# Kernel tuning notes

Measured on AMD Instinct MI355X. Metric: run time of the kernel, lower is better.

## Reference

```python
import jax, jax.numpy as jnp
import numpy as np

EPS = 1e-9
# ((top,bottom),(left,right)) zero-pads for the 8 neighbor directions,
# matching torch nn.ZeroPad2d((l,r,t,b)) order gate1..gate8 in the source.
PADS = [((0, 2), (0, 2)), ((0, 2), (1, 1)), ((0, 2), (2, 0)),
        ((1, 1), (0, 2)), ((1, 1), (2, 0)),
        ((2, 0), (0, 2)), ((2, 0), (1, 1)), ((2, 0), (2, 0))]


def _pad8(x):
    # x: (B,H,W) -> (B,8,H+2,W+2): 8 directional zero-padded shifts
    return jnp.stack([jnp.pad(x, ((0, 0), tb, lr)) for tb, lr in PADS], axis=1)


def _affinity_normalization(guidance):
    # guidance: (B,8,H,W) -> gate_wb (B,8,H+2,W+2), gate_sum (B,H,W)
    gate_wb = jnp.stack(
        [jnp.pad(guidance[:, k], ((0, 0), tb, lr)) for k, (tb, lr) in enumerate(PADS)],
        axis=1)
    abs_weight = jnp.sum(jnp.abs(gate_wb), axis=1, keepdims=True)
    gate_wb = gate_wb / (abs_weight + EPS)
    gate_sum = jnp.sum(gate_wb, axis=1)[:, 1:-1, 1:-1]
    return gate_wb, gate_sum


def setup_inputs() -> dict:
    key = jax.random.key(0)
    k1, k2, k3, k4 = jax.random.split(key, 4)
    B, H, W = 2, 384, 1280
    guidance = jax.random.normal(k1, (B, 8, H, W), dtype=jnp.float32)
    blur_depth = jax.random.uniform(k2, (B, 1, H, W), dtype=jnp.float32) * 80.0
    valid = (jax.random.uniform(k3, (B, 1, H, W)) < 0.05).astype(jnp.float32)
    sparse_depth = valid * jax.random.uniform(k4, (B, 1, H, W), dtype=jnp.float32) * 80.0
    return {"guidance": guidance, "blur_depth": blur_depth,
            "sparse_depth": sparse_depth, "prop_time": 24}


def reference(guidance, blur_depth, sparse_depth, prop_time):
    # CSPN affinity-guided iterative propagation (norm_type='8sum')
    gate_wb, gate_sum = _affinity_normalization(guidance)
    raw = blur_depth[:, 0]                       # (B,H,W)
    sparse_mask = jnp.sign(sparse_depth[:, 0])   # (B,H,W), 1 where valid
    d = raw
    for _ in range(prop_time):
        # weighted sum over 8 padded neighbor shifts, then crop halo
        nws = jnp.sum(gate_wb * _pad8(d), axis=1)[:, 1:-1, 1:-1]
        d = (1.0 - gate_sum) * raw + nws
        d = (1.0 - sparse_mask) * d + sparse_mask * raw
    return d  # (B,H,W), matches result_depth.squeeze(1)
```

## Files before the change

### kernel.cpp

```cpp
#include <hip/hip_runtime.h>
#include <hip/hip_fp16.h>

static constexpr int Hh = 384;
static constexpr int Ww = 1280;
static constexpr int HW = Hh * Ww;
static constexpr int NPIX = 2 * HW;
static constexpr int TILE = 32;
static constexpr int S = 6;
static constexpr int R = TILE + 2 * S;
static constexpr int RR = R * R;
static constexpr int ISIDE = R - 2;
static constexpr int NINT = ISIDE * ISIDE;
static constexpr int BLOCK = 256;
static constexpr int PPQ = (RR + BLOCK - 1) / BLOCK;
static constexpr int PPI = (NINT + BLOCK - 1) / BLOCK;
static constexpr int TI = Hh / TILE;
static constexpr int TJ = Ww / TILE;
static constexpr int GRID = 2 * TI * TJ;
static constexpr int NXCD = 8;
static constexpr int CHUNK = GRID / NXCD;
static constexpr float EPSF = 1e-9f;

__device__ __constant__ int DI_c[8] = { 1, 1, 1, 0, 0, -1, -1, -1 };
__device__ __constant__ int DJ_c[8] = { 1, 0, -1, 1, -1, 1, 0, -1 };

__global__ void affinity_norm(const float* __restrict__ g,
                              const float* __restrict__ raw,
                              const float* __restrict__ sparse,
                              __half* __restrict__ wbuf,
                              float* __restrict__ cbuf) {
    int idx = blockIdx.x * blockDim.x + threadIdx.x;
    if (idx >= NPIX) return;
    int b = idx / HW;
    int r = idx - b * HW;
    int i = r / Ww;
    int j = r - i * Ww;

    const float* gb = g + (size_t)b * 8 * HW;
    float v[8];
    float a = EPSF;
#pragma unroll
    for (int k = 0; k < 8; k++) {
        int ii = i + DI_c[k], jj = j + DJ_c[k];
        float gv = 0.0f;
        if (ii >= 0 && ii < Hh && jj >= 0 && jj < Ww)
            gv = gb[k * HW + ii * Ww + jj];
        v[k] = gv;
        a += fabsf(gv);
    }
    float inv = 1.0f / a, gs = 0.0f;
#pragma unroll
    for (int k = 0; k < 8; k++) { v[k] *= inv; gs += v[k]; }

    float rawv = raw[idx];
    bool m = sparse[idx] > 0.0f;
    cbuf[idx] = m ? rawv : (1.0f - gs) * rawv;
    __half wv[8];
#pragma unroll
    for (int k = 0; k < 8; k++) wv[k] = __float2half(m ? 0.0f : v[k]);
    *(float4*)(wbuf + (size_t)idx * 8) = *(const float4*)wv;
}

__global__ __launch_bounds__(BLOCK, 4) void fused_steps(
    const __half* __restrict__ wbuf, const float* __restrict__ cbuf,
    const float* __restrict__ din, float* __restrict__ dout)
{
    __shared__ float sd[2][RR];

    const int tid = threadIdx.x;
    int bx = (blockIdx.x % NXCD) * CHUNK + blockIdx.x / NXCD;
    const int tj = bx % TJ; bx /= TJ;
    const int ti = bx % TI;
    const int b  = bx / TI;
    const int oi = ti * TILE - S;
    const int oj = tj * TILE - S;

#pragma unroll
    for (int q = 0; q < PPQ; q++) {
        int p = tid + q * BLOCK;
        if (p < RR) {
            int ri = p / R, rj = p - ri * R;
            int gic = min(max(oi + ri, 0), Hh - 1);
            int gjc = min(max(oj + rj, 0), Ww - 1);
            float v = din[b * HW + gic * Ww + gjc];
            sd[0][p] = v;
            if (ri == 0 || ri == R - 1 || rj == 0 || rj == R - 1)
                sd[1][p] = v;
        }
    }

    float w[PPI][8];
    float C[PPI];
    int   pp[PPI];
    int   rng[PPI];
#pragma unroll
    for (int q = 0; q < PPI; q++) {
        int pi = tid + q * BLOCK;
        if (pi < NINT) {
            int r0 = pi / ISIDE;
            int ri = 1 + r0, rj = 1 + (pi - r0 * ISIDE);
            int p = ri * R + rj;
            pp[q]  = p;
            rng[q] = min(min(ri, R - 1 - ri), min(rj, R - 1 - rj));
            int gic = min(max(oi + ri, 0), Hh - 1);
            int gjc = min(max(oj + rj, 0), Ww - 1);
            int idx = b * HW + gic * Ww + gjc;
            float4 wv = *(const float4*)(wbuf + (size_t)idx * 8);
            const __half2* wh = (const __half2*)&wv;
            float2 w01 = __half22float2(wh[0]);
            float2 w23 = __half22float2(wh[1]);
            float2 w45 = __half22float2(wh[2]);
            float2 w67 = __half22float2(wh[3]);
            w[q][0] = w01.x; w[q][1] = w01.y; w[q][2] = w23.x; w[q][3] = w23.y;
            w[q][4] = w45.x; w[q][5] = w45.y; w[q][6] = w67.x; w[q][7] = w67.y;
            C[q] = cbuf[idx];
        } else {
            rng[q] = 0;
            pp[q] = 0;
        }
    }
    __syncthreads();

    int cur = 0;
#pragma unroll
    for (int s = 1; s < S; s++) {
        const float* s0 = sd[cur];
        float* s1 = sd[cur ^ 1];
#pragma unroll
        for (int q = 0; q < PPI; q++) {
            if (rng[q] >= s) {
                int p = pp[q];
                float v = C[q]
                    + w[q][0] * s0[p + R + 1] + w[q][1] * s0[p + R]
                    + w[q][2] * s0[p + R - 1] + w[q][3] * s0[p + 1]
                    + w[q][4] * s0[p - 1]     + w[q][5] * s0[p - R + 1]
                    + w[q][6] * s0[p - R]     + w[q][7] * s0[p - R - 1];
                s1[p] = v;
            }
        }
        __syncthreads();
        cur ^= 1;
    }

    const float* s0 = sd[cur];
#pragma unroll
    for (int q = 0; q < PPI; q++) {
        if (rng[q] >= S) {
            int p = pp[q];
            float v = C[q]
                + w[q][0] * s0[p + R + 1] + w[q][1] * s0[p + R]
                + w[q][2] * s0[p + R - 1] + w[q][3] * s0[p + 1]
                + w[q][4] * s0[p - 1]     + w[q][5] * s0[p - R + 1]
                + w[q][6] * s0[p - R]     + w[q][7] * s0[p - R - 1];
            int ri = p / R, rj = p - ri * R;
            dout[b * HW + (oi + ri) * Ww + (oj + rj)] = v;
        }
    }
}

extern "C" void kernel_launch(void* const* d_in, const int* in_sizes, int n_in,
                              void* d_out, int out_size, void* d_ws, size_t ws_size,
                              hipStream_t stream) {
    const float* guidance = (const float*)d_in[0];
    const float* blur     = (const float*)d_in[1];
    const float* sparse   = (const float*)d_in[2];
    float* out = (float*)d_out;

    char* ws = (char*)d_ws;
    float* bufA = (float*)ws;
    float* bufB = bufA + NPIX;
    __half* wbuf = (__half*)(bufB + NPIX);
    float*  cbuf = (float*)(wbuf + (size_t)NPIX * 8);

    const int threads = 256;
    const int blocks = (NPIX + threads - 1) / threads;
    affinity_norm<<<blocks, threads, 0, stream>>>(guidance, blur, sparse, wbuf, cbuf);

    fused_steps<<<GRID, BLOCK, 0, stream>>>(wbuf, cbuf, blur, bufA);
    fused_steps<<<GRID, BLOCK, 0, stream>>>(wbuf, cbuf, bufA, bufB);
    fused_steps<<<GRID, BLOCK, 0, stream>>>(wbuf, cbuf, bufB, bufA);
    fused_steps<<<GRID, BLOCK, 0, stream>>>(wbuf, cbuf, bufA, out);
}
```

Measured before the change: 142.5 us.

## Fuse affinity normalization and all propagation steps into one halo-tiled kernel

Replaces the separate affinity-normalization kernel and four 6-step propagation launches with a single kernel. Each block computes a 64x64 output tile with a 24-pixel halo entirely in shared memory. Each block computes its normalized weights directly from guidance, and it runs all 24 iterations without global intermediate buffers or relaunches. The cost is much more redundant halo compute, 512-thread blocks holding 24 pixels of packed-half weights per thread (heavy register pressure and likely spills), and low occupancy from the roughly 100 KB shared-memory footprint. The XCD block remapping is also dropped.

```diff
diff --git a/kernel.cpp b/kernel.cpp
--- a/kernel.cpp
+++ b/kernel.cpp
@@ -4,137 +4,122 @@
 static constexpr int Hh = 384;
 static constexpr int Ww = 1280;
 static constexpr int HW = Hh * Ww;
-static constexpr int NPIX = 2 * HW;
-static constexpr int TILE = 32;
-static constexpr int S = 6;
-static constexpr int R = TILE + 2 * S;
+static constexpr int TILE = 64;
+static constexpr int T = 24;
+static constexpr int R = TILE + 2 * T;
 static constexpr int RR = R * R;
 static constexpr int ISIDE = R - 2;
 static constexpr int NINT = ISIDE * ISIDE;
-static constexpr int BLOCK = 256;
+static constexpr int BLOCK = 512;
 static constexpr int PPQ = (RR + BLOCK - 1) / BLOCK;
 static constexpr int PPI = (NINT + BLOCK - 1) / BLOCK;
 static constexpr int TI = Hh / TILE;
 static constexpr int TJ = Ww / TILE;
 static constexpr int GRID = 2 * TI * TJ;
-static constexpr int NXCD = 8;
-static constexpr int CHUNK = GRID / NXCD;
 static constexpr float EPSF = 1e-9f;
 
-__device__ __constant__ int DI_c[8] = { 1, 1, 1, 0, 0, -1, -1, -1 };
-__device__ __constant__ int DJ_c[8] = { 1, 0, -1, 1, -1, 1, 0, -1 };
+static constexpr int DI[8] = { 1, 1, 1, 0, 0, -1, -1, -1 };
+static constexpr int DJ[8] = { 1, 0, -1, 1, -1, 1, 0, -1 };
 
-__global__ void affinity_norm(const float* __restrict__ g,
-                              const float* __restrict__ raw,
-                              const float* __restrict__ sparse,
-                              __half* __restrict__ wbuf,
-                              float* __restrict__ cbuf) {
-    int idx = blockIdx.x * blockDim.x + threadIdx.x;
-    if (idx >= NPIX) return;
-    int b = idx / HW;
-    int r = idx - b * HW;
-    int i = r / Ww;
-    int j = r - i * Ww;
-
-    const float* gb = g + (size_t)b * 8 * HW;
-    float v[8];
-    float a = EPSF;
-#pragma unroll
-    for (int k = 0; k < 8; k++) {
-        int ii = i + DI_c[k], jj = j + DJ_c[k];
-        float gv = 0.0f;
-        if (ii >= 0 && ii < Hh && jj >= 0 && jj < Ww)
-            gv = gb[k * HW + ii * Ww + jj];
-        v[k] = gv;
-        a += fabsf(gv);
-    }
-    float inv = 1.0f / a, gs = 0.0f;
-#pragma unroll
-    for (int k = 0; k < 8; k++) { v[k] *= inv; gs += v[k]; }
-
-    float rawv = raw[idx];
-    bool m = sparse[idx] > 0.0f;
-    cbuf[idx] = m ? rawv : (1.0f - gs) * rawv;
-    __half wv[8];
-#pragma unroll
-    for (int k = 0; k < 8; k++) wv[k] = __float2half(m ? 0.0f : v[k]);
-    *(float4*)(wbuf + (size_t)idx * 8) = *(const float4*)wv;
+static __device__ __forceinline__ int iclamp(int v, int lo, int hi) {
+    return min(max(v, lo), hi);
 }
 
-__global__ __launch_bounds__(BLOCK, 4) void fused_steps(
-    const __half* __restrict__ wbuf, const float* __restrict__ cbuf,
-    const float* __restrict__ din, float* __restrict__ dout)
+__global__ __launch_bounds__(BLOCK, 2) void mega(
+    const float* __restrict__ g,
+    const float* __restrict__ blur,
+    const float* __restrict__ sparse,
+    float* __restrict__ out)
 {
     __shared__ float sd[2][RR];
 
     const int tid = threadIdx.x;
-    int bx = (blockIdx.x % NXCD) * CHUNK + blockIdx.x / NXCD;
+    int bx = blockIdx.x;
     const int tj = bx % TJ; bx /= TJ;
     const int ti = bx % TI;
     const int b  = bx / TI;
-    const int oi = ti * TILE - S;
-    const int oj = tj * TILE - S;
+    const int oi = ti * TILE - T;
+    const int oj = tj * TILE - T;
+
+    const float* blurb = blur + (size_t)b * HW;
+    const float* gb    = g    + (size_t)b * 8 * HW;
 
 #pragma unroll
     for (int q = 0; q < PPQ; q++) {
         int p = tid + q * BLOCK;
         if (p < RR) {
             int ri = p / R, rj = p - ri * R;
-            int gic = min(max(oi + ri, 0), Hh - 1);
-            int gjc = min(max(oj + rj, 0), Ww - 1);
-            float v = din[b * HW + gic * Ww + gjc];
-            sd[0][p] = v;
-            if (ri == 0 || ri == R - 1 || rj == 0 || rj == R - 1)
-                sd[1][p] = v;
+            int gi = iclamp(oi + ri, 0, Hh - 1);
+            int gj = iclamp(oj + rj, 0, Ww - 1);
+            sd[0][p] = blurb[gi * Ww + gj];
         }
     }
 
-    float w[PPI][8];
-    float C[PPI];
-    int   pp[PPI];
-    int   rng[PPI];
+    __half2 wh[PPI][4];
+    float   Cc[PPI];
+    int     pp[PPI];
+    int     rng[PPI];
 #pragma unroll
     for (int q = 0; q < PPI; q++) {
         int pi = tid + q * BLOCK;
         if (pi < NINT) {
             int r0 = pi / ISIDE;
             int ri = 1 + r0, rj = 1 + (pi - r0 * ISIDE);
-            int p = ri * R + rj;
-            pp[q]  = p;
+            pp[q]  = ri * R + rj;
             rng[q] = min(min(ri, R - 1 - ri), min(rj, R - 1 - rj));
-            int gic = min(max(oi + ri, 0), Hh - 1);
-            int gjc = min(max(oj + rj, 0), Ww - 1);
-            int idx = b * HW + gic * Ww + gjc;
-            float4 wv = *(const float4*)(wbuf + (size_t)idx * 8);
-            const __half2* wh = (const __half2*)&wv;
-            float2 w01 = __half22float2(wh[0]);
-            float2 w23 = __half22float2(wh[1]);
-            float2 w45 = __half22float2(wh[2]);
-            float2 w67 = __half22float2(wh[3]);
-            w[q][0] = w01.x; w[q][1] = w01.y; w[q][2] = w23.x; w[q][3] = w23.y;
-            w[q][4] = w45.x; w[q][5] = w45.y; w[q][6] = w67.x; w[q][7] = w67.y;
-            C[q] = cbuf[idx];
+            int gi = iclamp(oi + ri, 0, Hh - 1);
+            int gj = iclamp(oj + rj, 0, Ww - 1);
+            float v[8];
+            float a = EPSF;
+#pragma unroll
+            for (int k = 0; k < 8; k++) {
+                int ii = gi + DI[k], jj = gj + DJ[k];
+                float gv = 0.0f;
+                if (ii >= 0 && ii < Hh && jj >= 0 && jj < Ww)
+                    gv = gb[k * HW + ii * Ww + jj];
+                v[k] = gv;
+                a += fabsf(gv);
+            }
+            float inv = 1.0f / a, gs = 0.0f;
+#pragma unroll
+            for (int k = 0; k < 8; k++) { v[k] *= inv; gs += v[k]; }
+            int idx = gi * Ww + gj;
+            float rawv = blurb[idx];
+            bool m = sparse[b * HW + idx] > 0.0f;
+            Cc[q] = m ? rawv : (1.0f - gs) * rawv;
+#pragma unroll
+            for (int k = 0; k < 4; k++) {
+                __half2 h;
+                h.x = __float2half(m ? 0.0f : v[2 * k]);
+                h.y = __float2half(m ? 0.0f : v[2 * k + 1]);
+                wh[q][k] = h;
+            }
         } else {
-            rng[q] = 0;
-            pp[q] = 0;
+            pp[q] = 0; rng[q] = 0; Cc[q] = 0.0f;
+#pragma unroll
+            for (int k = 0; k < 4; k++) wh[q][k] = __floats2half2_rn(0.0f, 0.0f);
         }
     }
     __syncthreads();
 
     int cur = 0;
-#pragma unroll
-    for (int s = 1; s < S; s++) {
+#pragma unroll 1
+    for (int s = 1; s < T; ++s) {
         const float* s0 = sd[cur];
         float* s1 = sd[cur ^ 1];
 #pragma unroll
         for (int q = 0; q < PPI; q++) {
             if (rng[q] >= s) {
                 int p = pp[q];
-                float v = C[q]
-                    + w[q][0] * s0[p + R + 1] + w[q][1] * s0[p + R]
-                    + w[q][2] * s0[p + R - 1] + w[q][3] * s0[p + 1]
-                    + w[q][4] * s0[p - 1]     + w[q][5] * s0[p - R + 1]
-                    + w[q][6] * s0[p - R]     + w[q][7] * s0[p - R - 1];
+                float2 w01 = __half22float2(wh[q][0]);
+                float2 w23 = __half22float2(wh[q][1]);
+                float2 w45 = __half22float2(wh[q][2]);
+                float2 w67 = __half22float2(wh[q][3]);
+                float v = Cc[q]
+                    + w01.x * s0[p + R + 1] + w01.y * s0[p + R]
+                    + w23.x * s0[p + R - 1] + w23.y * s0[p + 1]
+                    + w45.x * s0[p - 1]     + w45.y * s0[p - R + 1]
+                    + w67.x * s0[p - R]     + w67.y * s0[p - R - 1];
                 s1[p] = v;
             }
         }
@@ -145,15 +130,19 @@
     const float* s0 = sd[cur];
 #pragma unroll
     for (int q = 0; q < PPI; q++) {
-        if (rng[q] >= S) {
+        if (rng[q] >= T) {
             int p = pp[q];
-            float v = C[q]
-                + w[q][0] * s0[p + R + 1] + w[q][1] * s0[p + R]
-                + w[q][2] * s0[p + R - 1] + w[q][3] * s0[p + 1]
-                + w[q][4] * s0[p - 1]     + w[q][5] * s0[p - R + 1]
-                + w[q][6] * s0[p - R]     + w[q][7] * s0[p - R - 1];
+            float2 w01 = __half22float2(wh[q][0]);
+            float2 w23 = __half22float2(wh[q][1]);
+            float2 w45 = __half22float2(wh[q][2]);
+            float2 w67 = __half22float2(wh[q][3]);
+            float v = Cc[q]
+                + w01.x * s0[p + R + 1] + w01.y * s0[p + R]
+                + w23.x * s0[p + R - 1] + w23.y * s0[p + 1]
+                + w45.x * s0[p - 1]     + w45.y * s0[p - R + 1]
+                + w67.x * s0[p - R]     + w67.y * s0[p - R - 1];
             int ri = p / R, rj = p - ri * R;
-            dout[b * HW + (oi + ri) * Ww + (oj + rj)] = v;
+            out[b * HW + (oi + ri) * Ww + (oj + rj)] = v;
         }
     }
 }
@@ -166,18 +155,5 @@
     const float* sparse   = (const float*)d_in[2];
     float* out = (float*)d_out;
 
-    char* ws = (char*)d_ws;
-    float* bufA = (float*)ws;
-    float* bufB = bufA + NPIX;
-    __half* wbuf = (__half*)(bufB + NPIX);
-    float*  cbuf = (float*)(wbuf + (size_t)NPIX * 8);
-
-    const int threads = 256;
-    const int blocks = (NPIX + threads - 1) / threads;
-    affinity_norm<<<blocks, threads, 0, stream>>>(guidance, blur, sparse, wbuf, cbuf);
-
-    fused_steps<<<GRID, BLOCK, 0, stream>>>(wbuf, cbuf, blur, bufA);
-    fused_steps<<<GRID, BLOCK, 0, stream>>>(wbuf, cbuf, bufA, bufB);
-    fused_steps<<<GRID, BLOCK, 0, stream>>>(wbuf, cbuf, bufB, bufA);
-    fused_steps<<<GRID, BLOCK, 0, stream>>>(wbuf, cbuf, bufA, out);
+    mega<<<GRID, BLOCK, 0, stream>>>(guidance, blur, sparse, out);
 }
```

New measurement: 229.7 us. 61.1% more time.
